# Optimization experiments

Hardware: AMD Instinct MI355X
Metric: run time of the kernel (lower is better)

## Reference

```python
import jax, jax.numpy as jnp
import numpy as np
import math

HIDDEN = 2048
N_HEADS = 16
HEAD = HIDDEN // N_HEADS
B, S = 2, 2048


def setup_inputs() -> dict:
    key = jax.random.key(0)
    k1, k2, k3 = jax.random.split(key, 3)
    scale = 1.0 / math.sqrt(HIDDEN)
    return {
        "x": jax.random.normal(k1, (B, S, HIDDEN), dtype=jnp.float32),
        "w_qkv": jax.random.normal(k2, (HIDDEN, 3 * HIDDEN), dtype=jnp.float32) * scale,
        "b_qkv": jnp.zeros((3 * HIDDEN,), dtype=jnp.float32),
        "w_out": jax.random.normal(k3, (HIDDEN, HIDDEN), dtype=jnp.float32) * scale,
        "b_out": jnp.zeros((HIDDEN,), dtype=jnp.float32),
    }


def reference(x, w_qkv, b_qkv, w_out, b_out):
    b, s, _ = x.shape
    qkv = x @ w_qkv + b_qkv                      # [b, s, 3*hidden]
    q, k, v = jnp.split(qkv, 3, axis=-1)
    # 'b n (h l) -> b h n l'
    def heads(t):
        return t.reshape(b, s, N_HEADS, HEAD).transpose(0, 2, 1, 3)
    q, k, v = heads(q), heads(k), heads(v)
    scores = jnp.einsum("bhql,bhkl->bhqk", q, k) / math.sqrt(HEAD)
    # causal mask: positions where q_ind < k_ind get -10000 (matches source)
    q_ind = jnp.arange(s)[:, None]
    k_ind = jnp.arange(s)[None, :]
    scores = jnp.where(q_ind < k_ind, jnp.float32(-10000.0), scores)
    probs = jax.nn.softmax(scores, axis=-1)
    combined = jnp.einsum("bhqk,bhkl->bhql", probs, v)
    # 'b h q l -> b q (h l)'
    combined = combined.transpose(0, 2, 1, 3).reshape(b, s, HIDDEN)
    return combined @ w_out + b_out
```

## Files before the change

### kernel.cpp

```cpp
#include <hip/hip_runtime.h>
#include <hip/hip_bf16.h>

typedef __attribute__((ext_vector_type(4))) float f32x4;
typedef __attribute__((ext_vector_type(16))) float f32x16;
typedef __attribute__((ext_vector_type(8))) short bf16x8;

#define GBL_AS(p) (const __attribute__((address_space(1))) void*)(p)
#define LDS_AS(p) (__attribute__((address_space(3))) void*)(p)

__device__ __forceinline__ void gload_lds16(const void* g, void* l) {
  __builtin_amdgcn_global_load_lds(GBL_AS(g), LDS_AS(l), 16, 0, 0);
}

__device__ __forceinline__ ushort f2bf(float f) {
  union { float f; unsigned int u; } v; v.f = f;
  unsigned int r = v.u + 0x7fffu + ((v.u >> 16) & 1u);
  return (ushort)(r >> 16);
}

__global__ void prep_kernel(const float4* __restrict__ x4,
                            ushort4* __restrict__ xb4,
                            const float* __restrict__ wqkv,
                            ushort* __restrict__ wqkvt) {
  __shared__ float tile[64][65];
  const int blk = blockIdx.x;
  if (blk < 8192) {
    int i = blk * 256 + threadIdx.x;
    float4 v = x4[i];
    ushort4 o;
    o.x = f2bf(v.x); o.y = f2bf(v.y); o.z = f2bf(v.z); o.w = f2bf(v.w);
    xb4[i] = o;
  } else {
    const int idx = blk - 8192;
    const int bx = idx % 96, by = idx / 96;
    const int C = 6144, R = 2048;
    int tx = threadIdx.x & 63, ty = threadIdx.x >> 6;
    int r0 = by * 64, c0 = bx * 64;
#pragma unroll
    for (int i = 0; i < 64; i += 4)
      tile[ty + i][tx] = wqkv[(size_t)(r0 + ty + i) * C + (c0 + tx)];
    __syncthreads();
#pragma unroll
    for (int i = 0; i < 64; i += 4)
      wqkvt[(size_t)(c0 + ty + i) * R + (r0 + tx)] = f2bf(tile[tx][ty + i]);
  }
}

__global__ void transpose_cast_kernel(const float* __restrict__ in,
                                      ushort* __restrict__ out, int R, int C) {
  __shared__ float tile[64][65];
  int tx = threadIdx.x & 63, ty = threadIdx.x >> 6;
  int r0 = blockIdx.y * 64, c0 = blockIdx.x * 64;
#pragma unroll
  for (int i = 0; i < 64; i += 4)
    tile[ty + i][tx] = in[(size_t)(r0 + ty + i) * C + (c0 + tx)];
  __syncthreads();
#pragma unroll
  for (int i = 0; i < 64; i += 4)
    out[(size_t)(c0 + ty + i) * R + (r0 + tx)] = f2bf(tile[tx][ty + i]);
}

template <int MODE>
__global__ __launch_bounds__(256, 2) void gemm_bt_kernel(
    const ushort* __restrict__ A, const ushort* __restrict__ Bt,
    const float* __restrict__ bias, float* __restrict__ C,
    ushort* __restrict__ Qo, ushort* __restrict__ Ko, ushort* __restrict__ Vo,
    int M, int N, int K) {
  __shared__ ushort As[128 * 64];
  __shared__ ushort Bs[128 * 64];
  const int tid = threadIdx.x;
  const int w = tid >> 6, l = tid & 63;
  const int wr = w >> 1, wc = w & 1;
  const int m0 = blockIdx.y * 128, n0 = blockIdx.x * 128;

  f32x4 acc[4][4] = {};

  const int lr = l >> 3;
  const int lc = (l & 7) ^ lr;

  for (int k0 = 0; k0 < K; k0 += 64) {
#pragma unroll
    for (int i = 0; i < 4; ++i) {
      int row = i * 32 + w * 8 + lr;
      gload_lds16(A + (size_t)(m0 + row) * K + k0 + lc * 8,
                  (char*)As + (i * 32 + w * 8) * 128);
      gload_lds16(Bt + (size_t)(n0 + row) * K + k0 + lc * 8,
                  (char*)Bs + (i * 32 + w * 8) * 128);
    }
    __syncthreads();
    const char* Ab = (const char*)As;
    const char* Bb = (const char*)Bs;
#pragma unroll
    for (int ks = 0; ks < 2; ++ks) {
      bf16x8 af[4], bfr[4];
      int cc = ks * 4 + (l >> 4);
#pragma unroll
      for (int mi = 0; mi < 4; ++mi) {
        int row = wr * 64 + mi * 16 + (l & 15);
        af[mi] = *(const bf16x8*)(Ab + row * 128 + ((cc ^ (row & 7)) << 4));
      }
#pragma unroll
      for (int ni = 0; ni < 4; ++ni) {
        int row = wc * 64 + ni * 16 + (l & 15);
        bfr[ni] = *(const bf16x8*)(Bb + row * 128 + ((cc ^ (row & 7)) << 4));
      }
#pragma unroll
      for (int mi = 0; mi < 4; ++mi)
#pragma unroll
        for (int ni = 0; ni < 4; ++ni)
          acc[mi][ni] = __builtin_amdgcn_mfma_f32_16x16x32_bf16(
              af[mi], bfr[ni], acc[mi][ni], 0, 0, 0);
    }
    __syncthreads();
  }

  if (MODE == 0) {
#pragma unroll
    for (int mi = 0; mi < 4; ++mi) {
      int row = m0 + wr * 64 + mi * 16 + ((l >> 4) << 2);
#pragma unroll
      for (int ni = 0; ni < 4; ++ni) {
        int col = n0 + wc * 64 + ni * 16 + (l & 15);
        float b = bias[col];
#pragma unroll
        for (int r = 0; r < 4; ++r)
          C[(size_t)(row + r) * N + col] = acc[mi][ni][r] + b;
      }
    }
  } else {
    const float qscale = 0.08838834764831845f * 1.4426950408889634f;
#pragma unroll
    for (int ni = 0; ni < 4; ++ni) {
      int n = n0 + wc * 64 + ni * 16 + (l & 15);
      int which = n >> 11;
      int cc2 = n & 2047;
      int h = cc2 >> 7, d = cc2 & 127;
      float b = bias[n];
#pragma unroll
      for (int mi = 0; mi < 4; ++mi) {
        int m = m0 + wr * 64 + mi * 16 + ((l >> 4) << 2);
        int bb = m >> 11, s = m & 2047;
        int bh = bb * 16 + h;
        if (which == 0) {
#pragma unroll
          for (int r = 0; r < 4; ++r)
            Qo[((size_t)bh * 2048 + s + r) * 128 + d] =
                f2bf((acc[mi][ni][r] + b) * qscale);
        } else if (which == 1) {
#pragma unroll
          for (int r = 0; r < 4; ++r)
            Ko[((size_t)bh * 2048 + s + r) * 128 + d] = f2bf(acc[mi][ni][r] + b);
        } else {
          ushort4 pk;
          pk.x = f2bf(acc[mi][ni][0] + b);
          pk.y = f2bf(acc[mi][ni][1] + b);
          pk.z = f2bf(acc[mi][ni][2] + b);
          pk.w = f2bf(acc[mi][ni][3] + b);
          *(ushort4*)(Vo + ((size_t)bh * 128 + d) * 2048 + s) = pk;
        }
      }
    }
  }
}

__global__ __launch_bounds__(512, 2) void attn_kernel(
    const ushort* __restrict__ Qg, const ushort* __restrict__ Kg,
    const ushort* __restrict__ Vtg, ushort* __restrict__ Og) {
  constexpr int S = 2048, D = 128;
  __shared__ ushort Kl[2][128 * 128];
  __shared__ ushort Vl[2][128 * 128];

  const int tid = threadIdx.x, w = tid >> 6, l = tid & 63;
  const int lid = blockIdx.x;
  const int bh = lid & 31;
  const int j = lid >> 5;
  const int g = w >> 2, wv = w & 3;
  const int qb = (g == 0) ? (8 + j) : (7 - j);
  const int wq0 = qb * 128 + wv * 32;
  const int nt_blk = 9 + j;
  const int ql = l & 31, h32 = l >> 5;

  const ushort* Qb = Qg + (size_t)bh * S * D;
  const ushort* Kb = Kg + (size_t)bh * S * D;
  const ushort* Vb = Vtg + (size_t)bh * D * S;

  bf16x8 qf[8];
#pragma unroll
  for (int ks = 0; ks < 8; ++ks)
    qf[ks] = *(const bf16x8*)(Qb + (size_t)(wq0 + ql) * D + ks * 16 + h32 * 8);

  f32x16 o[4];
#pragma unroll
  for (int dt = 0; dt < 4; ++dt) o[dt] = 0.f;
  float mrun = -1e30f, lrun = 0.f;

  auto stage = [&](int t, int buf) {
    const int k0 = t * 128;
#pragma unroll
    for (int s2 = 0; s2 < 4; ++s2) {
      int i = w * 4 + s2;
      int row = i * 4 + (l >> 4);
      int ck = (l & 15) ^ (row & 7);
      gload_lds16(Kb + (size_t)(k0 + row) * D + ck * 8,
                  (char*)Kl[buf] + i * 1024);
    }
#pragma unroll
    for (int s2 = 0; s2 < 4; ++s2) {
      int i = w * 4 + s2;
      int row = i * 4 + (l >> 4);
      int ck = (l & 15) ^ (row & 7);
      gload_lds16(Vb + (size_t)row * S + k0 + ck * 8,
                  (char*)Vl[buf] + i * 1024);
    }
  };

  stage(0, 0);

  for (int t = 0; t < nt_blk; ++t) {
    const int cur = t & 1;
    const int k0 = t * 128;
    if (t + 1 < nt_blk) {
      stage(t + 1, cur ^ 1);
      asm volatile("s_waitcnt vmcnt(8)" ::: "memory");
    } else {
      asm volatile("s_waitcnt vmcnt(0)" ::: "memory");
    }
    __builtin_amdgcn_s_barrier();

    if (k0 < wq0 + 32) {
      const char* Kc = (const char*)Kl[cur];
      const char* Vc = (const char*)Vl[cur];
      const int swz0 = ql & 7;

      f32x16 sa[4];
#pragma unroll
      for (int kt = 0; kt < 4; ++kt) sa[kt] = 0.f;
#pragma unroll
      for (int p = 0; p < 2; ++p) {
        bf16x8 kf0[8], kf1[8];
        const char* base0 = Kc + (p * 64 + ql) * 256;
        const char* base1 = Kc + (p * 64 + 32 + ql) * 256;
#pragma unroll
        for (int ks = 0; ks < 8; ++ks) {
          int c = 2 * ks + h32;
          kf0[ks] = *(const bf16x8*)(base0 + ((c ^ swz0) << 4));
          kf1[ks] = *(const bf16x8*)(base1 + ((c ^ swz0) << 4));
        }
        __builtin_amdgcn_s_setprio(1);
#pragma unroll
        for (int ks = 0; ks < 8; ++ks) {
          sa[p * 2] = __builtin_amdgcn_mfma_f32_32x32x16_bf16(
              kf0[ks], qf[ks], sa[p * 2], 0, 0, 0);
          sa[p * 2 + 1] = __builtin_amdgcn_mfma_f32_32x32x16_bf16(
              kf1[ks], qf[ks], sa[p * 2 + 1], 0, 0, 0);
        }
        __builtin_amdgcn_s_setprio(0);
      }

      if (k0 + 127 > wq0) {
        int qq = wq0 + ql;
#pragma unroll
        for (int kt = 0; kt < 4; ++kt) {
          int kb = k0 + kt * 32 + 4 * h32;
#pragma unroll
          for (int rr = 0; rr < 16; ++rr) {
            int kk = kb + (rr & 3) + 8 * (rr >> 2);
            if (qq < kk) sa[kt][rr] = -1e9f;
          }
        }
      }

      float tmax = -1e30f;
#pragma unroll
      for (int kt = 0; kt < 4; ++kt)
#pragma unroll
        for (int rr = 0; rr < 16; ++rr) tmax = fmaxf(tmax, sa[kt][rr]);
      tmax = fmaxf(tmax, __shfl_xor(tmax, 32));

      if (!__all(tmax <= mrun + 11.5f)) {
        float mnew = fmaxf(mrun, tmax);
        float e = __builtin_amdgcn_exp2f(mrun - mnew);
        lrun *= e;
        mrun = mnew;
#pragma unroll
        for (int dt = 0; dt < 4; ++dt) o[dt] *= e;
      }

      float rsum = 0.f;
#pragma unroll
      for (int kt = 0; kt < 4; ++kt)
#pragma unroll
        for (int rr = 0; rr < 16; ++rr) {
          float p = __builtin_amdgcn_exp2f(sa[kt][rr] - mrun);
          sa[kt][rr] = p;
          rsum += p;
        }
      rsum += __shfl_xor(rsum, 32);
      lrun += rsum;

#pragma unroll
      for (int kt = 0; kt < 4; ++kt) {
#pragma unroll
        for (int u2 = 0; u2 < 2; ++u2) {
          int c = 4 * kt + 2 * u2 + h32;
          bf16x8 vf[4];
#pragma unroll
          for (int dt = 0; dt < 4; ++dt) {
            int row = dt * 32 + ql;
            vf[dt] = *(const bf16x8*)(Vc + row * 256 + ((c ^ swz0) << 4));
          }
          int A0, B0, A1, B1;
          asm("v_cvt_pk_bf16_f32 %0, %1, %2"
              : "=v"(A0) : "v"(sa[kt][u2 * 8 + 0]), "v"(sa[kt][u2 * 8 + 1]));
          asm("v_cvt_pk_bf16_f32 %0, %1, %2"
              : "=v"(B0) : "v"(sa[kt][u2 * 8 + 2]), "v"(sa[kt][u2 * 8 + 3]));
          asm("v_cvt_pk_bf16_f32 %0, %1, %2"
              : "=v"(A1) : "v"(sa[kt][u2 * 8 + 4]), "v"(sa[kt][u2 * 8 + 5]));
          asm("v_cvt_pk_bf16_f32 %0, %1, %2"
              : "=v"(B1) : "v"(sa[kt][u2 * 8 + 6]), "v"(sa[kt][u2 * 8 + 7]));
          auto r02 = __builtin_amdgcn_permlane32_swap(A0, A1, false, false);
          auto r13 = __builtin_amdgcn_permlane32_swap(B0, B1, false, false);
          union { int i[4]; bf16x8 v; } pu;
          pu.i[0] = r02[0];
          pu.i[1] = r13[0];
          pu.i[2] = r02[1];
          pu.i[3] = r13[1];
          __builtin_amdgcn_s_setprio(1);
#pragma unroll
          for (int dt = 0; dt < 4; ++dt)
            o[dt] = __builtin_amdgcn_mfma_f32_32x32x16_bf16(vf[dt], pu.v, o[dt],
                                                            0, 0, 0);
          __builtin_amdgcn_s_setprio(0);
        }
      }
    }
    asm volatile("s_waitcnt lgkmcnt(0)" ::: "memory");
    __builtin_amdgcn_s_barrier();
  }

  const int b = bh >> 4, h = bh & 15;
  float inv = 1.0f / lrun;
  size_t rowbase = ((size_t)b * 2048 + (wq0 + ql)) * 2048 + h * 128;
#pragma unroll
  for (int dt = 0; dt < 4; ++dt)
#pragma unroll
    for (int r4 = 0; r4 < 4; ++r4) {
      int col = dt * 32 + r4 * 8 + h32 * 4;
      ushort4 pk;
      pk.x = f2bf(o[dt][r4 * 4 + 0] * inv);
      pk.y = f2bf(o[dt][r4 * 4 + 1] * inv);
      pk.z = f2bf(o[dt][r4 * 4 + 2] * inv);
      pk.w = f2bf(o[dt][r4 * 4 + 3] * inv);
      *(ushort4*)(Og + rowbase + col) = pk;
    }
}

extern "C" void kernel_launch(void* const* d_in, const int* in_sizes, int n_in,
                              void* d_out, int out_size, void* d_ws,
                              size_t ws_size, hipStream_t stream) {
  const float* x = (const float*)d_in[0];
  const float* w_qkv = (const float*)d_in[1];
  const float* b_qkv = (const float*)d_in[2];
  const float* w_out = (const float*)d_in[3];
  const float* b_out = (const float*)d_in[4];
  float* out = (float*)d_out;
  char* ws = (char*)d_ws;

  if (ws_size < 92274688u) return;
  ushort* xb = (ushort*)(ws);
  ushort* wqkvt = (ushort*)(ws + 16777216);
  ushort* Q = (ushort*)(ws + 41943040);
  ushort* Kb = (ushort*)(ws + 58720256);
  ushort* Vt = (ushort*)(ws + 75497472);
  ushort* comb = xb;
  ushort* woutt = wqkvt;

  prep_kernel<<<dim3(11264), 256, 0, stream>>>((const float4*)x, (ushort4*)xb,
                                               w_qkv, wqkvt);
  gemm_bt_kernel<1><<<dim3(48, 32), 256, 0, stream>>>(
      xb, wqkvt, b_qkv, nullptr, Q, Kb, Vt, 4096, 6144, 2048);
  transpose_cast_kernel<<<dim3(32, 32), 256, 0, stream>>>(w_out, woutt, 2048,
                                                          2048);
  attn_kernel<<<dim3(256), 512, 0, stream>>>(Q, Kb, Vt, comb);
  gemm_bt_kernel<0><<<dim3(16, 32), 256, 0, stream>>>(
      comb, woutt, b_out, out, nullptr, nullptr, nullptr, 4096, 2048, 2048);
}
```

Baseline: 221.3 us.

## Process two 32-row query subtiles per wave in attention, halving waves per block

Each attention wave now handles 64 query rows (two 32-row subtiles) instead of 32, and the block shrinks from 8 to 4 waves. Each K fragment loaded from LDS feeds two MFMAs, halving LDS reads of K and V per unit of compute. Each wave issues twice as many global-to-LDS loads and the wait count is adjusted to match. The cost is roughly doubled register pressure for accumulators and Q fragments, and half as many waves per CU to hide latency, with only 256 blocks on the GPU.

```diff
diff --git a/kernel.cpp b/kernel.cpp
--- a/kernel.cpp
+++ b/kernel.cpp
@@ -163,7 +163,7 @@
   }
 }
 
-__global__ __launch_bounds__(512, 2) void attn_kernel(
+__global__ __launch_bounds__(256, 1) void attn_kernel(
     const ushort* __restrict__ Qg, const ushort* __restrict__ Kg,
     const ushort* __restrict__ Vtg, ushort* __restrict__ Og) {
   constexpr int S = 2048, D = 128;
@@ -174,9 +174,9 @@
   const int lid = blockIdx.x;
   const int bh = lid & 31;
   const int j = lid >> 5;
-  const int g = w >> 2, wv = w & 3;
+  const int g = w >> 1, wv = w & 1;
   const int qb = (g == 0) ? (8 + j) : (7 - j);
-  const int wq0 = qb * 128 + wv * 32;
+  const int wq0 = qb * 128 + wv * 64;
   const int nt_blk = 9 + j;
   const int ql = l & 31, h32 = l >> 5;
 
@@ -184,29 +184,34 @@
   const ushort* Kb = Kg + (size_t)bh * S * D;
   const ushort* Vb = Vtg + (size_t)bh * D * S;
 
-  bf16x8 qf[8];
-#pragma unroll
-  for (int ks = 0; ks < 8; ++ks)
-    qf[ks] = *(const bf16x8*)(Qb + (size_t)(wq0 + ql) * D + ks * 16 + h32 * 8);
-
-  f32x16 o[4];
-#pragma unroll
-  for (int dt = 0; dt < 4; ++dt) o[dt] = 0.f;
-  float mrun = -1e30f, lrun = 0.f;
+  bf16x8 qf[2][8];
+#pragma unroll
+  for (int r = 0; r < 2; ++r)
+#pragma unroll
+    for (int ks = 0; ks < 8; ++ks)
+      qf[r][ks] = *(const bf16x8*)(Qb + (size_t)(wq0 + r * 32 + ql) * D +
+                                   ks * 16 + h32 * 8);
+
+  f32x16 o[2][4];
+#pragma unroll
+  for (int r = 0; r < 2; ++r)
+#pragma unroll
+    for (int dt = 0; dt < 4; ++dt) o[r][dt] = 0.f;
+  float mrun[2] = {-1e30f, -1e30f}, lrun[2] = {0.f, 0.f};
 
   auto stage = [&](int t, int buf) {
     const int k0 = t * 128;
 #pragma unroll
-    for (int s2 = 0; s2 < 4; ++s2) {
-      int i = w * 4 + s2;
+    for (int s2 = 0; s2 < 8; ++s2) {
+      int i = w * 8 + s2;
       int row = i * 4 + (l >> 4);
       int ck = (l & 15) ^ (row & 7);
       gload_lds16(Kb + (size_t)(k0 + row) * D + ck * 8,
                   (char*)Kl[buf] + i * 1024);
     }
 #pragma unroll
-    for (int s2 = 0; s2 < 4; ++s2) {
-      int i = w * 4 + s2;
+    for (int s2 = 0; s2 < 8; ++s2) {
+      int i = w * 8 + s2;
       int row = i * 4 + (l >> 4);
       int ck = (l & 15) ^ (row & 7);
       gload_lds16(Vb + (size_t)row * S + k0 + ck * 8,
@@ -221,20 +226,22 @@
     const int k0 = t * 128;
     if (t + 1 < nt_blk) {
       stage(t + 1, cur ^ 1);
-      asm volatile("s_waitcnt vmcnt(8)" ::: "memory");
+      asm volatile("s_waitcnt vmcnt(16)" ::: "memory");
     } else {
       asm volatile("s_waitcnt vmcnt(0)" ::: "memory");
     }
     __builtin_amdgcn_s_barrier();
 
-    if (k0 < wq0 + 32) {
+    if (k0 < wq0 + 64) {
       const char* Kc = (const char*)Kl[cur];
       const char* Vc = (const char*)Vl[cur];
       const int swz0 = ql & 7;
 
-      f32x16 sa[4];
-#pragma unroll
-      for (int kt = 0; kt < 4; ++kt) sa[kt] = 0.f;
+      f32x16 sa[2][4];
+#pragma unroll
+      for (int r = 0; r < 2; ++r)
+#pragma unroll
+        for (int kt = 0; kt < 4; ++kt) sa[r][kt] = 0.f;
 #pragma unroll
       for (int p = 0; p < 2; ++p) {
         bf16x8 kf0[8], kf1[8];
@@ -249,54 +256,62 @@
         __builtin_amdgcn_s_setprio(1);
 #pragma unroll
         for (int ks = 0; ks < 8; ++ks) {
-          sa[p * 2] = __builtin_amdgcn_mfma_f32_32x32x16_bf16(
-              kf0[ks], qf[ks], sa[p * 2], 0, 0, 0);
-          sa[p * 2 + 1] = __builtin_amdgcn_mfma_f32_32x32x16_bf16(
-              kf1[ks], qf[ks], sa[p * 2 + 1], 0, 0, 0);
+          sa[0][p * 2] = __builtin_amdgcn_mfma_f32_32x32x16_bf16(
+              kf0[ks], qf[0][ks], sa[0][p * 2], 0, 0, 0);
+          sa[1][p * 2] = __builtin_amdgcn_mfma_f32_32x32x16_bf16(
+              kf0[ks], qf[1][ks], sa[1][p * 2], 0, 0, 0);
+          sa[0][p * 2 + 1] = __builtin_amdgcn_mfma_f32_32x32x16_bf16(
+              kf1[ks], qf[0][ks], sa[0][p * 2 + 1], 0, 0, 0);
+          sa[1][p * 2 + 1] = __builtin_amdgcn_mfma_f32_32x32x16_bf16(
+              kf1[ks], qf[1][ks], sa[1][p * 2 + 1], 0, 0, 0);
         }
         __builtin_amdgcn_s_setprio(0);
       }
 
-      if (k0 + 127 > wq0) {
-        int qq = wq0 + ql;
-#pragma unroll
-        for (int kt = 0; kt < 4; ++kt) {
-          int kb = k0 + kt * 32 + 4 * h32;
+#pragma unroll
+      for (int r = 0; r < 2; ++r) {
+        const int sq0 = wq0 + r * 32;
+        if (k0 + 127 > sq0) {
+          int qq = sq0 + ql;
+#pragma unroll
+          for (int kt = 0; kt < 4; ++kt) {
+            int kb = k0 + kt * 32 + 4 * h32;
+#pragma unroll
+            for (int rr = 0; rr < 16; ++rr) {
+              int kk = kb + (rr & 3) + 8 * (rr >> 2);
+              if (qq < kk) sa[r][kt][rr] = -1e9f;
+            }
+          }
+        }
+
+        float tmax = -1e30f;
+#pragma unroll
+        for (int kt = 0; kt < 4; ++kt)
+#pragma unroll
+          for (int rr = 0; rr < 16; ++rr) tmax = fmaxf(tmax, sa[r][kt][rr]);
+        tmax = fmaxf(tmax, __shfl_xor(tmax, 32));
+
+        if (!__all(tmax <= mrun[r] + 11.5f)) {
+          float mnew = fmaxf(mrun[r], tmax);
+          float e = __builtin_amdgcn_exp2f(mrun[r] - mnew);
+          lrun[r] *= e;
+          mrun[r] = mnew;
+#pragma unroll
+          for (int dt = 0; dt < 4; ++dt) o[r][dt] *= e;
+        }
+
+        float rsum = 0.f;
+#pragma unroll
+        for (int kt = 0; kt < 4; ++kt)
 #pragma unroll
           for (int rr = 0; rr < 16; ++rr) {
-            int kk = kb + (rr & 3) + 8 * (rr >> 2);
-            if (qq < kk) sa[kt][rr] = -1e9f;
+            float p = __builtin_amdgcn_exp2f(sa[r][kt][rr] - mrun[r]);
+            sa[r][kt][rr] = p;
+            rsum += p;
           }
-        }
-      }
-
-      float tmax = -1e30f;
-#pragma unroll
-      for (int kt = 0; kt < 4; ++kt)
-#pragma unroll
-        for (int rr = 0; rr < 16; ++rr) tmax = fmaxf(tmax, sa[kt][rr]);
-      tmax = fmaxf(tmax, __shfl_xor(tmax, 32));
-
-      if (!__all(tmax <= mrun + 11.5f)) {
-        float mnew = fmaxf(mrun, tmax);
-        float e = __builtin_amdgcn_exp2f(mrun - mnew);
-        lrun *= e;
-        mrun = mnew;
-#pragma unroll
-        for (int dt = 0; dt < 4; ++dt) o[dt] *= e;
-      }
-
-      float rsum = 0.f;
-#pragma unroll
-      for (int kt = 0; kt < 4; ++kt)
-#pragma unroll
-        for (int rr = 0; rr < 16; ++rr) {
-          float p = __builtin_amdgcn_exp2f(sa[kt][rr] - mrun);
-          sa[kt][rr] = p;
-          rsum += p;
-        }
-      rsum += __shfl_xor(rsum, 32);
-      lrun += rsum;
+        rsum += __shfl_xor(rsum, 32);
+        lrun[r] += rsum;
+      }
 
 #pragma unroll
       for (int kt = 0; kt < 4; ++kt) {
@@ -309,28 +324,31 @@
             int row = dt * 32 + ql;
             vf[dt] = *(const bf16x8*)(Vc + row * 256 + ((c ^ swz0) << 4));
           }
-          int A0, B0, A1, B1;
-          asm("v_cvt_pk_bf16_f32 %0, %1, %2"
-              : "=v"(A0) : "v"(sa[kt][u2 * 8 + 0]), "v"(sa[kt][u2 * 8 + 1]));
-          asm("v_cvt_pk_bf16_f32 %0, %1, %2"
-              : "=v"(B0) : "v"(sa[kt][u2 * 8 + 2]), "v"(sa[kt][u2 * 8 + 3]));
-          asm("v_cvt_pk_bf16_f32 %0, %1, %2"
-              : "=v"(A1) : "v"(sa[kt][u2 * 8 + 4]), "v"(sa[kt][u2 * 8 + 5]));
-          asm("v_cvt_pk_bf16_f32 %0, %1, %2"
-              : "=v"(B1) : "v"(sa[kt][u2 * 8 + 6]), "v"(sa[kt][u2 * 8 + 7]));
-          auto r02 = __builtin_amdgcn_permlane32_swap(A0, A1, false, false);
-          auto r13 = __builtin_amdgcn_permlane32_swap(B0, B1, false, false);
-          union { int i[4]; bf16x8 v; } pu;
-          pu.i[0] = r02[0];
-          pu.i[1] = r13[0];
-          pu.i[2] = r02[1];
-          pu.i[3] = r13[1];
-          __builtin_amdgcn_s_setprio(1);
-#pragma unroll
-          for (int dt = 0; dt < 4; ++dt)
-            o[dt] = __builtin_amdgcn_mfma_f32_32x32x16_bf16(vf[dt], pu.v, o[dt],
-                                                            0, 0, 0);
-          __builtin_amdgcn_s_setprio(0);
+#pragma unroll
+          for (int r = 0; r < 2; ++r) {
+            int A0, B0, A1, B1;
+            asm("v_cvt_pk_bf16_f32 %0, %1, %2"
+                : "=v"(A0) : "v"(sa[r][kt][u2 * 8 + 0]), "v"(sa[r][kt][u2 * 8 + 1]));
+            asm("v_cvt_pk_bf16_f32 %0, %1, %2"
+                : "=v"(B0) : "v"(sa[r][kt][u2 * 8 + 2]), "v"(sa[r][kt][u2 * 8 + 3]));
+            asm("v_cvt_pk_bf16_f32 %0, %1, %2"
+                : "=v"(A1) : "v"(sa[r][kt][u2 * 8 + 4]), "v"(sa[r][kt][u2 * 8 + 5]));
+            asm("v_cvt_pk_bf16_f32 %0, %1, %2"
+                : "=v"(B1) : "v"(sa[r][kt][u2 * 8 + 6]), "v"(sa[r][kt][u2 * 8 + 7]));
+            auto r02 = __builtin_amdgcn_permlane32_swap(A0, A1, false, false);
+            auto r13 = __builtin_amdgcn_permlane32_swap(B0, B1, false, false);
+            union { int i[4]; bf16x8 v; } pu;
+            pu.i[0] = r02[0];
+            pu.i[1] = r13[0];
+            pu.i[2] = r02[1];
+            pu.i[3] = r13[1];
+            __builtin_amdgcn_s_setprio(1);
+#pragma unroll
+            for (int dt = 0; dt < 4; ++dt)
+              o[r][dt] = __builtin_amdgcn_mfma_f32_32x32x16_bf16(
+                  vf[dt], pu.v, o[r][dt], 0, 0, 0);
+            __builtin_amdgcn_s_setprio(0);
+          }
         }
       }
     }
@@ -339,20 +357,23 @@
   }
 
   const int b = bh >> 4, h = bh & 15;
-  float inv = 1.0f / lrun;
-  size_t rowbase = ((size_t)b * 2048 + (wq0 + ql)) * 2048 + h * 128;
-#pragma unroll
-  for (int dt = 0; dt < 4; ++dt)
-#pragma unroll
-    for (int r4 = 0; r4 < 4; ++r4) {
-      int col = dt * 32 + r4 * 8 + h32 * 4;
-      ushort4 pk;
-      pk.x = f2bf(o[dt][r4 * 4 + 0] * inv);
-      pk.y = f2bf(o[dt][r4 * 4 + 1] * inv);
-      pk.z = f2bf(o[dt][r4 * 4 + 2] * inv);
-      pk.w = f2bf(o[dt][r4 * 4 + 3] * inv);
-      *(ushort4*)(Og + rowbase + col) = pk;
-    }
+#pragma unroll
+  for (int r = 0; r < 2; ++r) {
+    float inv = 1.0f / lrun[r];
+    size_t rowbase = ((size_t)b * 2048 + (wq0 + r * 32 + ql)) * 2048 + h * 128;
+#pragma unroll
+    for (int dt = 0; dt < 4; ++dt)
+#pragma unroll
+      for (int r4 = 0; r4 < 4; ++r4) {
+        int col = dt * 32 + r4 * 8 + h32 * 4;
+        ushort4 pk;
+        pk.x = f2bf(o[r][dt][r4 * 4 + 0] * inv);
+        pk.y = f2bf(o[r][dt][r4 * 4 + 1] * inv);
+        pk.z = f2bf(o[r][dt][r4 * 4 + 2] * inv);
+        pk.w = f2bf(o[r][dt][r4 * 4 + 3] * inv);
+        *(ushort4*)(Og + rowbase + col) = pk;
+      }
+  }
 }
 
 extern "C" void kernel_launch(void* const* d_in, const int* in_sizes, int n_in,
@@ -381,7 +402,7 @@
       xb, wqkvt, b_qkv, nullptr, Q, Kb, Vt, 4096, 6144, 2048);
   transpose_cast_kernel<<<dim3(32, 32), 256, 0, stream>>>(w_out, woutt, 2048,
                                                           2048);
-  attn_kernel<<<dim3(256), 512, 0, stream>>>(Q, Kb, Vt, comb);
+  attn_kernel<<<dim3(256), 256, 0, stream>>>(Q, Kb, Vt, comb);
   gemm_bt_kernel<0><<<dim3(16, 32), 256, 0, stream>>>(
       comb, woutt, b_out, out, nullptr, nullptr, nullptr, 4096, 2048, 2048);
 }
```

New measurement: 368.5 us. +66.6%, slower.
